# Kernel optimization log

Measured on AMD Instinct MI355X. Metric: run time of the kernel, lower is better.

## Reference

```python
import jax, jax.numpy as jnp
import numpy as np

B, S, H, UNITS = 32, 2048, 1024, 1024

def setup_inputs() -> dict:
    key = jax.random.key(0)
    ks = jax.random.split(key, 8)
    sc_h = 1.0 / np.sqrt(H)
    sc_u = 1.0 / np.sqrt(UNITS)
    return {
        "query": jax.random.normal(ks[0], (B, H), jnp.float32),
        "values": jax.random.normal(ks[1], (B, S, H), jnp.float32),
        "W1": jax.random.normal(ks[2], (H, UNITS), jnp.float32) * sc_h,
        "b1": jnp.zeros((UNITS,), jnp.float32),
        "W2": jax.random.normal(ks[3], (H, UNITS), jnp.float32) * sc_h,
        "b2": jnp.zeros((UNITS,), jnp.float32),
        "V": jax.random.normal(ks[4], (UNITS, 1), jnp.float32) * sc_u,
        "bv": jnp.zeros((1,), jnp.float32),
    }

def reference(query, values, W1, b1, W2, b2, V, bv):
    # W1(values): [B,S,U]; W2(query)[:,None,:]: [B,1,U] broadcast-added
    proj = jnp.tanh(
        jnp.einsum("bsh,hu->bsu", values, W1) + b1
        + (query @ W2 + b2)[:, None, :]
    )
    score = proj @ V + bv                      # [B,S,1]
    attention_weights = jax.nn.softmax(score, axis=1)  # softmax over seq
    context_vector = jnp.sum(attention_weights * values, axis=1)  # [B,H]
    return context_vector, attention_weights
```

## Files before the change

### kernel.cpp

```cpp
#include <hip/hip_runtime.h>
#include <hip/hip_bf16.h>


#define B_ 32
#define S_ 2048
#define H_ 1024
#define U_ 1024
#define M_ (B_ * S_)

typedef __bf16 bf16;
typedef __bf16 bf16x8 __attribute__((ext_vector_type(8)));
typedef float  f32x4  __attribute__((ext_vector_type(4)));

__device__ __forceinline__ void gl2lds16(const void* g, void* l) {
    __builtin_amdgcn_global_load_lds(
        (const __attribute__((address_space(1))) void*)g,
        (__attribute__((address_space(3))) void*)l, 16, 0, 0);
}

__device__ __forceinline__ bf16x8 cvt8(float4 a, float4 b) {
    bf16x8 o;
    o[0] = (bf16)a.x; o[1] = (bf16)a.y; o[2] = (bf16)a.z; o[3] = (bf16)a.w;
    o[4] = (bf16)b.x; o[5] = (bf16)b.y; o[6] = (bf16)b.z; o[7] = (bf16)b.w;
    return o;
}

__global__ void prep_kernel(const float* __restrict__ W1, bf16* __restrict__ W1T,
                            const float* __restrict__ query, const float* __restrict__ W2,
                            const float* __restrict__ b2, float* __restrict__ q2) {
    __shared__ __align__(16) char smem[64 * 65 * 2];
    int tid = threadIdx.x;
    if (blockIdx.x < 256) {
        bf16* t = (bf16*)smem;
        int h0 = (blockIdx.x >> 4) * 64, u0 = (blockIdx.x & 15) * 64;
        #pragma unroll
        for (int i = 0; i < 16; ++i) {
            int idx = i * 256 + tid;
            int r = idx >> 6, c = idx & 63;
            t[c * 65 + r] = (bf16)W1[(long)(h0 + r) * U_ + u0 + c];
        }
        __syncthreads();
        #pragma unroll
        for (int i = 0; i < 16; ++i) {
            int idx = i * 256 + tid;
            int r = idx >> 6, c = idx & 63;
            W1T[(long)(u0 + r) * H_ + h0 + c] = t[r * 65 + c];
        }
    } else {
        float* qsh  = (float*)smem;
        float* part = (float*)(smem + 4096);
        int idx = blockIdx.x - 256;
        int b  = idx >> 4;
        int u0 = (idx & 15) * 64;
        int ul = tid & 63, kc = tid >> 6;
        for (int i = tid; i < H_; i += 256) qsh[i] = query[b * H_ + i];
        __syncthreads();
        float acc = 0.f;
        const float* wp = W2 + (long)(kc * 256) * U_ + u0 + ul;
        #pragma unroll 8
        for (int h = 0; h < 256; ++h) acc += qsh[kc * 256 + h] * wp[(long)h * U_];
        part[kc * 64 + ul] = acc;
        __syncthreads();
        if (tid < 64)
            q2[b * U_ + u0 + tid] = part[tid] + part[64 + tid] + part[128 + tid]
                                    + part[192 + tid] + b2[u0 + tid];
    }
}

#define ASTRIDE 40
__global__ __launch_bounds__(256, 3) void score_gemm(
    const float* __restrict__ A32,
    const bf16* __restrict__ BT,
    const float* __restrict__ b1, const float* __restrict__ q2,
    const float* __restrict__ V, float* __restrict__ score )
{
    __shared__ __align__(16) bf16 a_sh[2 * 128 * ASTRIDE];
    __shared__ __align__(16) bf16 b_sh[2 * 128 * 32];
    const int tid  = threadIdx.x;
    const int lane = tid & 63;
    const int wave = tid >> 6;
    const int wm = wave >> 1, wn = wave & 1;
    const int xcd = blockIdx.x & 7;
    const int i_  = blockIdx.x >> 3;
    const int nt  = i_ & 7;
    const int mt  = xcd * 64 + (i_ >> 3);
    const long m0 = (long)mt * 128;
    const int  n0 = nt * 128;
    const int lrow = lane & 15;
    const int quad = lane >> 4;
    const int arow = tid >> 1;
    const int aseg = tid & 1;

    f32x4 acc[4][4];
    const f32x4 zero = {0.f, 0.f, 0.f, 0.f};
    #pragma unroll
    for (int mi = 0; mi < 4; ++mi)
        #pragma unroll
        for (int ni = 0; ni < 4; ++ni) acc[mi][ni] = zero;

    const float* Abase = A32 + m0 * H_;
    const bf16*  Bbase = BT + (long)n0 * H_;

    for (int kt = 0; kt < H_; kt += 64) {
        #pragma unroll
        for (int i = 0; i < 4; ++i) {
            int g  = i * 4 + wave;
            int hs = g >> 3, q = g & 7;
            int row = q * 16 + (lane >> 2);
            int gc  = (lane & 3) ^ ((row >> 1) & 3);
            gl2lds16(Bbase + (long)row * H_ + kt + hs * 32 + gc * 8,
                     (void*)(b_sh + hs * 4096 + q * 512));
        }
        float4 av[2][4];
        #pragma unroll
        for (int hs = 0; hs < 2; ++hs) {
            const float4* src = reinterpret_cast<const float4*>(
                Abase + (long)arow * H_ + kt + hs * 32 + aseg * 16);
            av[hs][0] = src[0]; av[hs][1] = src[1];
            av[hs][2] = src[2]; av[hs][3] = src[3];
        }
        #pragma unroll
        for (int hs = 0; hs < 2; ++hs) {
            bf16* dst = a_sh + hs * (128 * ASTRIDE) + arow * ASTRIDE + aseg * 16;
            *reinterpret_cast<bf16x8*>(dst)     = cvt8(av[hs][0], av[hs][1]);
            *reinterpret_cast<bf16x8*>(dst + 8) = cvt8(av[hs][2], av[hs][3]);
        }
        __syncthreads();

        #pragma unroll
        for (int hs = 0; hs < 2; ++hs) {
            bf16x8 af[4], bg[4];
            #pragma unroll
            for (int mi = 0; mi < 4; ++mi) {
                int r = wm * 64 + mi * 16 + lrow;
                af[mi] = *reinterpret_cast<const bf16x8*>(
                    a_sh + hs * (128 * ASTRIDE) + r * ASTRIDE + quad * 8);
            }
            #pragma unroll
            for (int ni = 0; ni < 4; ++ni) {
                int r = wn * 64 + ni * 16 + lrow;
                int p = quad ^ ((r >> 1) & 3);
                bg[ni] = *reinterpret_cast<const bf16x8*>(
                    b_sh + hs * 4096 + r * 32 + p * 8);
            }
            #pragma unroll
            for (int mi = 0; mi < 4; ++mi)
                #pragma unroll
                for (int ni = 0; ni < 4; ++ni)
                    acc[mi][ni] = __builtin_amdgcn_mfma_f32_16x16x32_bf16(
                        af[mi], bg[ni], acc[mi][ni], 0, 0, 0);
        }
        __syncthreads();
    }

    const int bb = (int)(m0 / S_);
    float bq[4], vv[4];
    #pragma unroll
    for (int ni = 0; ni < 4; ++ni) {
        int u = n0 + wn * 64 + ni * 16 + lrow;
        bq[ni] = b1[u] + q2[bb * U_ + u];
        vv[ni] = V[u];
    }
    #pragma unroll
    for (int mi = 0; mi < 4; ++mi) {
        #pragma unroll
        for (int r = 0; r < 4; ++r) {
            float s = 0.f;
            #pragma unroll
            for (int ni = 0; ni < 4; ++ni) {
                float x = acc[mi][ni][r] + bq[ni];
                float t = 1.f - 2.f / (__expf(2.f * x) + 1.f);
                s += t * vv[ni];
            }
            s += __shfl_xor(s, 1); s += __shfl_xor(s, 2);
            s += __shfl_xor(s, 4); s += __shfl_xor(s, 8);
            if (lrow == 0)
                atomicAdd(score + m0 + wm * 64 + mi * 16 + quad * 4 + r, s);
        }
    }
}

__global__ void softmax_kernel(float* __restrict__ attn) {
    __shared__ float sh[S_];
    __shared__ float red[8];
    int b = blockIdx.x, tid = threadIdx.x;
    float* row = attn + (long)b * S_;
    float lmax = -1e30f;
    for (int i = tid; i < S_; i += 256) { float v = row[i]; sh[i] = v; lmax = fmaxf(lmax, v); }
    #pragma unroll
    for (int m = 32; m; m >>= 1) lmax = fmaxf(lmax, __shfl_xor(lmax, m));
    if ((tid & 63) == 0) red[tid >> 6] = lmax;
    __syncthreads();
    float gmax = fmaxf(fmaxf(red[0], red[1]), fmaxf(red[2], red[3]));
    float lsum = 0.f;
    for (int i = tid; i < S_; i += 256) { float e = __expf(sh[i] - gmax); sh[i] = e; lsum += e; }
    #pragma unroll
    for (int m = 32; m; m >>= 1) lsum += __shfl_xor(lsum, m);
    if ((tid & 63) == 0) red[4 + (tid >> 6)] = lsum;
    __syncthreads();
    float inv = 1.f / (red[4] + red[5] + red[6] + red[7]);
    for (int i = tid; i < S_; i += 256) row[i] = sh[i] * inv;
}

__global__ void context_kernel(const float* __restrict__ vals, const float* __restrict__ attn,
                               float* __restrict__ ctx ) {
    __shared__ float a_sh[128];
    int b = blockIdx.x >> 4;
    int sc = blockIdx.x & 15;
    int tid = threadIdx.x;
    if (tid < 128) a_sh[tid] = attn[(long)b * S_ + sc * 128 + tid];
    __syncthreads();
    const float* base = vals + ((long)b * S_ + sc * 128) * H_ + tid * 4;
    float ax = 0.f, ay = 0.f, az = 0.f, aw = 0.f;
    #pragma unroll 4
    for (int s = 0; s < 128; ++s) {
        float w = a_sh[s];
        float4 v = *reinterpret_cast<const float4*>(base + (long)s * H_);
        ax += w * v.x; ay += w * v.y; az += w * v.z; aw += w * v.w;
    }
    float* c = ctx + (long)b * H_ + tid * 4;
    atomicAdd(c + 0, ax); atomicAdd(c + 1, ay);
    atomicAdd(c + 2, az); atomicAdd(c + 3, aw);
}

extern "C" void kernel_launch(void* const* d_in, const int* in_sizes, int n_in,
                              void* d_out, int out_size, void* d_ws, size_t ws_size,
                              hipStream_t stream) {
    const float* query  = (const float*)d_in[0];
    const float* values = (const float*)d_in[1];
    const float* W1     = (const float*)d_in[2];
    const float* b1     = (const float*)d_in[3];
    const float* W2     = (const float*)d_in[4];
    const float* b2     = (const float*)d_in[5];
    const float* V      = (const float*)d_in[6];

    char* ws = (char*)d_ws;
    bf16*  w1t = (bf16*)ws;
    float* q2  = (float*)(ws + (size_t)U_ * H_ * 2);

    float* ctx  = (float*)d_out;
    float* attn = (float*)d_out + B_ * H_;

    hipMemsetAsync(d_out, 0, (size_t)(B_ * H_ + B_ * S_) * sizeof(float), stream);

    prep_kernel   <<<768,            256, 0, stream>>>(W1, w1t, query, W2, b2, q2);
    score_gemm    <<<(M_ / 128) * 8, 256, 0, stream>>>(values, w1t, b1, q2, V, attn);
    softmax_kernel<<<B_,             256, 0, stream>>>(attn);
    context_kernel<<<B_ * 16,        256, 0, stream>>>(values, attn, ctx);
}
```

Baseline: 597.6 us.

## Pre-convert values to bf16 and use 256x256 direct-to-LDS pipelined GEMM

```diff
diff --git a/kernel.cpp b/kernel.cpp
--- a/kernel.cpp
+++ b/kernel.cpp
@@ -7,6 +7,7 @@
 #define H_ 1024
 #define U_ 1024
 #define M_ (B_ * S_)
+#define NT_ 32
 
 typedef __bf16 bf16;
 typedef __bf16 bf16x8 __attribute__((ext_vector_type(8)));
@@ -27,7 +28,8 @@
 
 __global__ void prep_kernel(const float* __restrict__ W1, bf16* __restrict__ W1T,
                             const float* __restrict__ query, const float* __restrict__ W2,
-                            const float* __restrict__ b2, float* __restrict__ q2) {
+                            const float* __restrict__ b2, float* __restrict__ q2,
+                            const float* __restrict__ values, bf16* __restrict__ vbf) {
     __shared__ __align__(16) char smem[64 * 65 * 2];
     int tid = threadIdx.x;
     if (blockIdx.x < 256) {
@@ -46,7 +48,7 @@
             int r = idx >> 6, c = idx & 63;
             W1T[(long)(u0 + r) * H_ + h0 + c] = t[r * 65 + c];
         }
-    } else {
+    } else if (blockIdx.x < 768) {
         float* qsh  = (float*)smem;
         float* part = (float*)(smem + 4096);
         int idx = blockIdx.x - 256;
@@ -64,6 +66,142 @@
         if (tid < 64)
             q2[b * U_ + u0 + tid] = part[tid] + part[64 + tid] + part[128 + tid]
                                     + part[192 + tid] + b2[u0 + tid];
+    } else {
+        long cid = (long)(blockIdx.x - 768) * 256 + tid;
+        const long stride = 4096L * 256;
+        const long n8 = (long)M_ * H_ / 8;
+        for (long c = cid; c < n8; c += stride) {
+            const float4* s = reinterpret_cast<const float4*>(values + c * 8);
+            float4 a = s[0], b = s[1];
+            *reinterpret_cast<bf16x8*>(vbf + c * 8) = cvt8(a, b);
+        }
+    }
+}
+
+__global__ __launch_bounds__(512, 2) void score_gemm8(
+    const bf16* __restrict__ A,
+    const bf16* __restrict__ BT,
+    const float* __restrict__ b1, const float* __restrict__ q2,
+    const float* __restrict__ V, float* __restrict__ score )
+{
+    __shared__ __align__(16) bf16 lds[65536];
+    const int tid  = threadIdx.x;
+    const int lane = tid & 63;
+    const int wave = tid >> 6;
+    const int wm = wave >> 2, wn = wave & 3;
+    const int lrow = lane & 15, quad = lane >> 4;
+
+    const int xcd = blockIdx.x & 7;
+    const int j   = blockIdx.x >> 3;
+    const int mt  = xcd * 32 + (j >> 2);
+    const int nt  = j & 3;
+    const long m0 = (long)mt * 256;
+    const int  n0 = nt * 256;
+
+    const int rs = wave * 16 + (lane >> 2);
+    const int sl = (lane & 3) ^ ((lane >> 3) & 3);
+    const bf16* a0  = A  + (m0 + rs) * H_ + sl * 8;
+    const bf16* a1  = a0 + 128 * H_;
+    const bf16* bt0 = BT + (long)(n0 + rs) * H_ + sl * 8;
+    const bf16* bt1 = bt0 + 128 * H_;
+
+    const int kse  = (quad ^ ((lrow >> 1) & 3)) * 8;
+    const int aoff = (wm * 128 + lrow) * 32 + kse;
+    const int boff = 8192 + (wn * 64 + lrow) * 32 + kse;
+
+    f32x4 acc[8][4];
+    const f32x4 zero = {0.f, 0.f, 0.f, 0.f};
+    #pragma unroll
+    for (int mi = 0; mi < 8; ++mi)
+        #pragma unroll
+        for (int ni = 0; ni < 4; ++ni) acc[mi][ni] = zero;
+
+    for (int tt = 0; tt < 3; ++tt) {
+        bf16* d = lds + tt * 16384 + wave * 512;
+        gl2lds16(a0  + tt * 32, d);
+        gl2lds16(a1  + tt * 32, d + 4096);
+        gl2lds16(bt0 + tt * 32, d + 8192);
+        gl2lds16(bt1 + tt * 32, d + 8192 + 4096);
+    }
+    __builtin_amdgcn_sched_barrier(0);
+    asm volatile("s_waitcnt vmcnt(8)" ::: "memory");
+    __builtin_amdgcn_s_barrier();
+    __builtin_amdgcn_sched_barrier(0);
+
+    #pragma unroll 1
+    for (int t = 0; t < NT_; ++t) {
+        const bf16* buf = lds + (t & 3) * 16384;
+        if (t + 3 < NT_) {
+            bf16* d = lds + ((t + 3) & 3) * 16384 + wave * 512;
+            gl2lds16(a0 + (t + 3) * 32, d);
+            gl2lds16(a1 + (t + 3) * 32, d + 4096);
+        }
+        bf16x8 af[4], bg[4];
+        #pragma unroll
+        for (int ni = 0; ni < 4; ++ni)
+            bg[ni] = *reinterpret_cast<const bf16x8*>(buf + boff + ni * 512);
+        #pragma unroll
+        for (int mi = 0; mi < 4; ++mi)
+            af[mi] = *reinterpret_cast<const bf16x8*>(buf + aoff + mi * 512);
+        __builtin_amdgcn_s_setprio(1);
+        #pragma unroll
+        for (int mi = 0; mi < 4; ++mi)
+            #pragma unroll
+            for (int ni = 0; ni < 4; ++ni)
+                acc[mi][ni] = __builtin_amdgcn_mfma_f32_16x16x32_bf16(
+                    af[mi], bg[ni], acc[mi][ni], 0, 0, 0);
+        __builtin_amdgcn_s_setprio(0);
+        __builtin_amdgcn_sched_barrier(0);
+        __builtin_amdgcn_s_barrier();
+        __builtin_amdgcn_sched_barrier(0);
+        if (t + 3 < NT_) {
+            bf16* d = lds + ((t + 3) & 3) * 16384 + 8192 + wave * 512;
+            gl2lds16(bt0 + (t + 3) * 32, d);
+            gl2lds16(bt1 + (t + 3) * 32, d + 4096);
+        }
+        #pragma unroll
+        for (int mi = 0; mi < 4; ++mi)
+            af[mi] = *reinterpret_cast<const bf16x8*>(buf + aoff + (4 + mi) * 512);
+        __builtin_amdgcn_s_setprio(1);
+        #pragma unroll
+        for (int mi = 0; mi < 4; ++mi)
+            #pragma unroll
+            for (int ni = 0; ni < 4; ++ni)
+                acc[4 + mi][ni] = __builtin_amdgcn_mfma_f32_16x16x32_bf16(
+                    af[mi], bg[ni], acc[4 + mi][ni], 0, 0, 0);
+        __builtin_amdgcn_s_setprio(0);
+        __builtin_amdgcn_sched_barrier(0);
+        if (t < NT_ - 3)       asm volatile("s_waitcnt vmcnt(8)" ::: "memory");
+        else if (t == NT_ - 3) asm volatile("s_waitcnt vmcnt(4)" ::: "memory");
+        else if (t == NT_ - 2) asm volatile("s_waitcnt vmcnt(0)" ::: "memory");
+        __builtin_amdgcn_s_barrier();
+        __builtin_amdgcn_sched_barrier(0);
+    }
+
+    const int bb = (int)(m0 / S_);
+    float bq[4], vv[4];
+    #pragma unroll
+    for (int ni = 0; ni < 4; ++ni) {
+        int u = n0 + wn * 64 + ni * 16 + lrow;
+        bq[ni] = b1[u] + q2[bb * U_ + u];
+        vv[ni] = V[u];
+    }
+    #pragma unroll
+    for (int mi = 0; mi < 8; ++mi) {
+        #pragma unroll
+        for (int r = 0; r < 4; ++r) {
+            float s = 0.f;
+            #pragma unroll
+            for (int ni = 0; ni < 4; ++ni) {
+                float x = acc[mi][ni][r] + bq[ni];
+                float th = 1.f - 2.f / (__expf(2.f * x) + 1.f);
+                s += th * vv[ni];
+            }
+            s += __shfl_xor(s, 1); s += __shfl_xor(s, 2);
+            s += __shfl_xor(s, 4); s += __shfl_xor(s, 8);
+            if (lrow == 0)
+                atomicAdd(score + m0 + wm * 128 + mi * 16 + quad * 4 + r, s);
+        }
     }
 }
 
@@ -237,14 +375,22 @@
     char* ws = (char*)d_ws;
     bf16*  w1t = (bf16*)ws;
     float* q2  = (float*)(ws + (size_t)U_ * H_ * 2);
+    bf16*  vbf = (bf16*)(ws + (size_t)U_ * H_ * 2 + (size_t)B_ * U_ * 4);
+    const size_t need = (size_t)U_ * H_ * 2 + (size_t)B_ * U_ * 4
+                      + (size_t)M_ * H_ * 2;
 
     float* ctx  = (float*)d_out;
     float* attn = (float*)d_out + B_ * H_;
 
     hipMemsetAsync(d_out, 0, (size_t)(B_ * H_ + B_ * S_) * sizeof(float), stream);
 
-    prep_kernel   <<<768,            256, 0, stream>>>(W1, w1t, query, W2, b2, q2);
-    score_gemm    <<<(M_ / 128) * 8, 256, 0, stream>>>(values, w1t, b1, q2, V, attn);
-    softmax_kernel<<<B_,             256, 0, stream>>>(attn);
-    context_kernel<<<B_ * 16,        256, 0, stream>>>(values, attn, ctx);
-}
+    if (ws_size >= need) {
+        prep_kernel <<<768 + 4096, 256, 0, stream>>>(W1, w1t, query, W2, b2, q2, values, vbf);
+        score_gemm8 <<<1024,       512, 0, stream>>>(vbf, w1t, b1, q2, V, attn);
+    } else {
+        prep_kernel <<<768,        256, 0, stream>>>(W1, w1t, query, W2, b2, q2, values, vbf);
+        score_gemm  <<<(M_ / 128) * 8, 256, 0, stream>>>(values, w1t, b1, q2, V, attn);
+    }
+    softmax_kernel<<<B_,      256, 0, stream>>>(attn);
+    context_kernel<<<B_ * 16, 256, 0, stream>>>(values, attn, ctx);
+}
```

Measured after the change: 609.7 us. 1.02x slower.
